# Kernel tuning notes

Measured on AMD Instinct MI355X. Metric: run time of the kernel, lower is better.

The kernel has to match this reference:

```python
import jax, jax.numpy as jnp
import numpy as np
from jax import lax

# ModifiedSRCMLayer dims
B, C, H, W = 4, 128, 64, 64
G, DM = 4, 32          # groups, d_model per group = input_dim // groups
DI, DS, DC = 64, 16, 4 # d_inner = expand*DM, d_state, d_conv
DTR = 2                # dt_rank = ceil(DM/16)
OUT = 128              # output_dim
PE_HW = 64             # sqrt(4096) pos_embed grid
EPS = 1e-5


def setup_inputs() -> dict:
    key = jax.random.key(0)
    ks = jax.random.split(key, 16)
    def n(k, shape, s=0.02):
        return jax.random.normal(k, shape, jnp.float32) * s
    inp = {}
    inp["x"] = jax.random.normal(ks[0], (B, C, H, W), jnp.float32)
    # ConvPosEnc: depthwise 3x3
    inp["pos_conv_w"] = n(ks[1], (C, 1, 3, 3))
    inp["pos_conv_b"] = jnp.zeros((C,), jnp.float32)
    inp["pos_embed"] = jax.random.normal(ks[2], (1, PE_HW * PE_HW, C), jnp.float32)  # torch.randn init
    inp["ln_g"] = jnp.ones((C,), jnp.float32)
    inp["ln_b"] = jnp.zeros((C,), jnp.float32)
    inp["gate_W"] = n(ks[3], (C, C))
    inp["gate_b"] = jnp.zeros((C,), jnp.float32)
    inp["proj_W"] = n(ks[4], (OUT, C))
    inp["proj_b"] = jnp.zeros((OUT,), jnp.float32)
    # per-group bidirectional Mamba (bimamba v2) params; axis0=group, axis1=direction
    inp["m_Win"] = n(ks[5], (G, 2 * DI, DM))
    inp["m_Wout"] = n(ks[6], (G, DM, DI))
    inp["conv_w"] = n(ks[7], (G, 2, DI, DC))
    inp["conv_b"] = jnp.zeros((G, 2, DI), jnp.float32)
    inp["xproj_W"] = n(ks[8], (G, 2, DTR + 2 * DS, DI))
    inp["dt_W"] = n(ks[9], (G, 2, DI, DTR), 0.1)
    inp["dt_b"] = n(ks[10], (G, 2, DI), 0.1)
    A = jnp.log(jnp.tile(jnp.arange(1, DS + 1, dtype=jnp.float32)[None, :], (DI, 1)))  # S4D-real init
    inp["A_log"] = jnp.tile(A[None, None], (G, 2, 1, 1))
    inp["Dskip"] = jnp.ones((G, 2, DI), jnp.float32)
    return inp


def _causal_dwconv(x, w, b):
    # x: (B,L,DI), w: (DI,DC) depthwise causal conv along L
    xt = x.transpose(0, 2, 1)  # (B,DI,L)
    y = lax.conv_general_dilated(xt, w[:, None, :], (1,), [(DC - 1, 0)],
                                 feature_group_count=DI,
                                 dimension_numbers=('NCH', 'OIH', 'NCH'))
    return (y + b[None, :, None]).transpose(0, 2, 1)


def _selective_scan(u, dt, Bm, Cm, A, D):
    # u, dt: (B,L,DI); Bm, Cm: (B,L,DS); A: (DI,DS); D: (DI,)
    def step(h, inp):
        u_t, dt_t, B_t, C_t = inp  # (B,DI),(B,DI),(B,DS),(B,DS)
        dA = jnp.exp(dt_t[:, :, None] * A)                       # (B,DI,DS)
        h = dA * h + (dt_t * u_t)[:, :, None] * B_t[:, None, :]
        return h, jnp.einsum('bds,bs->bd', h, C_t)
    xs = (u.transpose(1, 0, 2), dt.transpose(1, 0, 2),
          Bm.transpose(1, 0, 2), Cm.transpose(1, 0, 2))
    h0 = jnp.zeros((u.shape[0], DI, DS), u.dtype)
    _, ys = lax.scan(step, h0, xs)  # (L,B,DI)
    return ys.transpose(1, 0, 2) + u * D


def _mamba_dir(u, z, conv_w, conv_b, xproj_W, dt_W, dt_b, A_log, D):
    uc = jax.nn.silu(_causal_dwconv(u, conv_w, conv_b))
    dbl = uc @ xproj_W.T                                  # (B,L,DTR+2*DS)
    dt, Bm, Cm = jnp.split(dbl, [DTR, DTR + DS], axis=-1)
    dt = jax.nn.softplus(dt @ dt_W.T + dt_b)              # (B,L,DI)
    y = _selective_scan(uc, dt, Bm, Cm, -jnp.exp(A_log), D)
    return y * jax.nn.silu(z)


def _conv_mamba(xg, Win, Wout, conv_w, conv_b, xproj_W, dt_W, dt_b, A_log, D):
    # xg: (B,L,DM); bidirectional (bimamba v2): fwd scan + flipped scan, summed
    xz = xg @ Win.T
    u, z = jnp.split(xz, 2, axis=-1)
    yf = _mamba_dir(u, z, conv_w[0], conv_b[0], xproj_W[0], dt_W[0], dt_b[0], A_log[0], D[0])
    yb = _mamba_dir(u[:, ::-1], z[:, ::-1], conv_w[1], conv_b[1], xproj_W[1],
                    dt_W[1], dt_b[1], A_log[1], D[1])[:, ::-1]
    return (yf + yb) @ Wout.T


def reference(x, pos_conv_w, pos_conv_b, pos_embed, ln_g, ln_b, gate_W, gate_b,
              proj_W, proj_b, m_Win, m_Wout, conv_w, conv_b, xproj_W, dt_W,
              dt_b, A_log, Dskip):
    Bsz, Cc, Hh, Ww = x.shape
    L = Hh * Ww
    # ConvPosEnc: x + depthwise 3x3
    pe = lax.conv_general_dilated(x, pos_conv_w, (1, 1), [(1, 1), (1, 1)],
                                  feature_group_count=Cc,
                                  dimension_numbers=('NCHW', 'OIHW', 'NCHW'))
    x = x + pe + pos_conv_b[None, :, None, None]
    xs = x.reshape(Bsz, Cc, L).transpose(0, 2, 1)  # (B,L,C)
    # bilinear pos_embed interpolation (align_corners=False == half-pixel 'linear')
    pemb = pos_embed.transpose(0, 2, 1).reshape(1, Cc, PE_HW, PE_HW)
    pemb = jax.image.resize(pemb, (1, Cc, Hh, Ww), 'linear')
    xs = xs + pemb.reshape(1, Cc, L).transpose(0, 2, 1)
    # LayerNorm over channels
    mu = xs.mean(-1, keepdims=True)
    var = ((xs - mu) ** 2).mean(-1, keepdims=True)
    xn = (xs - mu) * lax.rsqrt(var + EPS) * ln_g + ln_b
    # split into G channel groups, run ConvMamba per group (vmapped)
    chunks = xn.reshape(Bsz, L, G, DM).transpose(2, 0, 1, 3)  # (G,B,L,DM)
    ym = jax.vmap(_conv_mamba)(chunks, m_Win, m_Wout, conv_w, conv_b,
                               xproj_W, dt_W, dt_b, A_log, Dskip)  # (G,B,L,DM)
    x_mamba = ym.transpose(1, 2, 0, 3).reshape(Bsz, L, Cc)
    gate = jax.nn.sigmoid(xn @ gate_W.T + gate_b)
    out = gate * x_mamba + (1.0 - gate) * xs
    out = out @ proj_W.T + proj_b
    return out.transpose(0, 2, 1).reshape(Bsz, OUT, Hh, Ww)
```

## Files before the change

kernel.cpp:

```cpp
#include <hip/hip_runtime.h>
#include <hip/hip_bf16.h>
#include <hip/hip_fp16.h>

#define NS 128
#define CL 32

__global__ __launch_bounds__(256) void k1a_conv(
    const float* __restrict__ x, const float* __restrict__ pcw,
    const float* __restrict__ pcb, const float* __restrict__ pemb,
    float* __restrict__ xs)
{
  const int h = blockIdx.x;
  const int b = blockIdx.y >> 2;
  const int c0 = (blockIdx.y & 3) * 32;
  const int tid = threadIdx.x;
  __shared__ float tile[32][65];
  for (int i = 0; i < 8; ++i) {
    int e = tid + 256*i;
    int c = e >> 6, w = e & 63;
    const float* xp = x + ((size_t)(b*128 + c0 + c))*4096;
    const float* wp = pcw + (c0 + c)*9;
    float acc = xp[h*64 + w] + pcb[c0 + c];
    #pragma unroll
    for (int dh = -1; dh <= 1; ++dh) {
      int hh = h + dh;
      if (hh < 0 || hh >= 64) continue;
      #pragma unroll
      for (int dw = -1; dw <= 1; ++dw) {
        int ww = w + dw;
        if (ww < 0 || ww >= 64) continue;
        acc += xp[hh*64 + ww] * wp[(dh+1)*3 + (dw+1)];
      }
    }
    tile[c][w] = acc;
  }
  __syncthreads();
  for (int i = 0; i < 8; ++i) {
    int e = tid + 256*i;
    int w = e >> 5, cc = e & 31;
    int l = h*64 + w;
    xs[((size_t)(b*4096 + l))*128 + c0 + cc] =
        tile[cc][w] + pemb[(size_t)l*128 + c0 + cc];
  }
}

__global__ __launch_bounds__(256) void k1b_ln(
    const float* __restrict__ xs, const float* __restrict__ lng,
    const float* __restrict__ lnb, float* __restrict__ xn)
{
  const int tid = threadIdx.x;
  const int r = tid >> 5, lane = tid & 31;
  const size_t row = (size_t)(blockIdx.x*8 + r);
  const size_t base = row*128 + lane*4;
  float4 v = *(const float4*)&xs[base];
  float sum = v.x + v.y + v.z + v.w;
  float ss  = v.x*v.x + v.y*v.y + v.z*v.z + v.w*v.w;
  sum += __shfl_xor(sum, 1);  ss += __shfl_xor(ss, 1);
  sum += __shfl_xor(sum, 2);  ss += __shfl_xor(ss, 2);
  sum += __shfl_xor(sum, 4);  ss += __shfl_xor(ss, 4);
  sum += __shfl_xor(sum, 8);  ss += __shfl_xor(ss, 8);
  sum += __shfl_xor(sum, 16); ss += __shfl_xor(ss, 16);
  float mu = sum * (1.f/128.f);
  float rs = rsqrtf(ss * (1.f/128.f) - mu*mu + 1e-5f);
  float4 g = *(const float4*)&lng[lane*4];
  float4 be = *(const float4*)&lnb[lane*4];
  float4 o;
  o.x = (v.x - mu)*rs*g.x + be.x;
  o.y = (v.y - mu)*rs*g.y + be.y;
  o.z = (v.z - mu)*rs*g.z + be.z;
  o.w = (v.w - mu)*rs*g.w + be.w;
  *(float4*)&xn[base] = o;
}

__global__ __launch_bounds__(256) void k23_xz_conv_xproj(
    const float* __restrict__ xn, const float* __restrict__ mWin,
    const float* __restrict__ convw, const float* __restrict__ convb,
    const float* __restrict__ xprojW,
    float* __restrict__ uc, float* __restrict__ dtB, float* __restrict__ Cb)
{
  const int l0 = blockIdx.x * 32;
  const int gb = blockIdx.y;
  const int g = gb >> 2, b = gb & 3;
  const int tid = threadIdx.x;
  const int d = tid & 63, t4 = tid >> 6;

  __shared__ float xn_s[38][36];
  __shared__ float u_s[38][68];
  __shared__ float uc_s[32][68];
  __shared__ float xw_s[34][68];

  for (int i = 0; i < 2; ++i) {
    int e = tid + 256*i;
    if (e < 304) {
      int rr = e >> 3, q = e & 7;
      int gr = l0 - 3 + rr;
      float4 v = make_float4(0.f, 0.f, 0.f, 0.f);
      if (gr >= 0 && gr < 4096)
        v = *(const float4*)&xn[((size_t)(b*4096 + gr))*128 + g*32 + q*4];
      *(float4*)&xn_s[rr][q*4] = v;
    }
  }
  float wu[32];
  {
    const float* wr = mWin + (size_t)(g*128 + d)*32;
    #pragma unroll
    for (int q = 0; q < 8; ++q)
      ((float4*)wu)[q] = *(const float4*)&wr[q*4];
  }
  __syncthreads();
  for (int ii = 0; ii < 10; ++ii) {
    int r = t4 + 4*ii;
    if (r < 38) {
      float au = 0.f;
      #pragma unroll
      for (int k4 = 0; k4 < 8; ++k4) {
        float4 a4 = *(const float4*)&xn_s[r][k4*4];
        float4 w4 = ((float4*)wu)[k4];
        au += a4.x*w4.x + a4.y*w4.y + a4.z*w4.z + a4.w*w4.w;
      }
      u_s[r][d] = au;
    }
  }

  for (int dir = 0; dir < 2; ++dir) {
    __syncthreads();
    {
      int g2 = g*2 + dir;
      float4 w4 = *(const float4*)&convw[(g2*64 + d)*4];
      float bb = convb[g2*64 + d];
      float* ucg = uc + ((size_t)(g2*4 + b)*4096)*64;
      #pragma unroll
      for (int ii = 0; ii < 8; ++ii) {
        int r = t4 + 4*ii;
        float acc;
        if (dir == 0)
          acc = bb + u_s[r  ][d]*w4.x + u_s[r+1][d]*w4.y
                   + u_s[r+2][d]*w4.z + u_s[r+3][d]*w4.w;
        else
          acc = bb + u_s[r+3][d]*w4.w + u_s[r+4][d]*w4.z
                   + u_s[r+5][d]*w4.y + u_s[r+6][d]*w4.x;
        acc = acc / (1.f + __expf(-acc));
        uc_s[r][d] = acc;
        int t = l0 + r;
        int tw = dir ? 4095 - t : t;
        ucg[(size_t)tw*64 + d] = acc;
      }
    }
    for (int i = 0; i < 3; ++i) {
      int e = tid + 256*i;
      if (e < 544) {
        int row = e >> 4, q = e & 15;
        *(float4*)&xw_s[row][q*4] =
          *(const float4*)&xprojW[((size_t)((g*2 + dir)*34 + row))*64 + q*4];
      }
    }
    __syncthreads();
    {
      const int rg = tid >> 3, cg = tid & 7;
      float acc[5] = {};
      #pragma unroll
      for (int k4 = 0; k4 < 16; ++k4) {
        float4 u0 = *(const float4*)&uc_s[rg][k4*4];
        #pragma unroll
        for (int j = 0; j < 4; ++j) {
          float4 w = *(const float4*)&xw_s[cg + 8*j][k4*4];
          acc[j] += u0.x*w.x + u0.y*w.y + u0.z*w.z + u0.w*w.w;
        }
        if (cg < 2) {
          float4 w = *(const float4*)&xw_s[32 + cg][k4*4];
          acc[4] += u0.x*w.x + u0.y*w.y + u0.z*w.z + u0.w*w.w;
        }
      }
      int gdb = (g*2 + dir)*4 + b;
      float* dtBg = dtB + ((size_t)gdb*4096)*20;
      float* Cbg  = Cb  + ((size_t)gdb*4096)*16;
      int t = l0 + rg;
      int tw = dir ? 4095 - t : t;
      #pragma unroll
      for (int j = 0; j < 4; ++j) {
        int c = cg + 8*j;
        if (c < 2)       dtBg[(size_t)tw*20 + c] = acc[j];
        else if (c < 18) dtBg[(size_t)tw*20 + 2 + c] = acc[j];
        else             Cbg[(size_t)tw*16 + (c - 18)] = acc[j];
      }
      if (cg < 2) Cbg[(size_t)tw*16 + 14 + cg] = acc[4];
    }
  }
}

__global__ __launch_bounds__(256) void k_scan1y(
    const float* __restrict__ dtB, const float* __restrict__ Cb,
    float* __restrict__ uc,
    const float* __restrict__ dtW, const float* __restrict__ dtb_,
    const float* __restrict__ Dsk, __half* __restrict__ ecum,
    float* __restrict__ hseed, float* __restrict__ eprod)
{
  const int chunk = blockIdx.x;
  const int gdb = blockIdx.y;
  const int g2 = gdb >> 2;
  const int tid = threadIdx.x;
  const int d = tid >> 2, sq = tid & 3, s0 = sq*4;
  const int dld = tid & 63;

  __shared__ float  E_s[2][8][64];
  __shared__ __align__(16) float2 duu_s[2][8][64];
  __shared__ __align__(16) float  bc_s[2][8][32];
  __shared__ float  y_st[2][8][64];
  __shared__ float  e_st[2][8][64];

  float* ucg = uc + ((size_t)gdb*4096)*64;
  const float* dtBg = dtB + ((size_t)gdb*4096)*20;
  const float* Cbg  = Cb  + ((size_t)gdb*4096)*16;
  const int base = chunk * CL;
  __half* eg = ecum + ((size_t)gdb*4096 + base)*64;

  const float dtw0 = dtW[(g2*64 + dld)*2 + 0];
  const float dtw1 = dtW[(g2*64 + dld)*2 + 1];
  const float dtbv = dtb_[g2*64 + dld];
  const float Dd = Dsk[g2*64 + d];

  float h0=0.f,h1=0.f,h2=0.f,h3=0.f, Ec=1.f;

  float pu0, pu1, pc;
  float2 pq0, pq1;
  auto issue = [&](int t0) {
    int ttA = tid >> 6;
    pu0 = ucg[(size_t)(t0+ttA)*64 + dld];
    pq0 = *(const float2*)&dtBg[(size_t)(t0+ttA)*20];
    pu1 = ucg[(size_t)(t0+ttA+4)*64 + dld];
    pq1 = *(const float2*)&dtBg[(size_t)(t0+ttA+4)*20];
    int col = tid & 31, row = t0 + (tid >> 5);
    pc = (col < 16) ? dtBg[(size_t)row*20 + 4 + col]
                    : Cbg[(size_t)row*16 + (col - 16)];
  };
  auto commit = [&](int buf) {
    int ttA = tid >> 6;
    #pragma unroll
    for (int half = 0; half < 2; ++half) {
      int tt = ttA + 4*half;
      float uu = half ? pu1 : pu0;
      float2 pq = half ? pq1 : pq0;
      float v = pq.x*dtw0 + pq.y*dtw1 + dtbv;
      float dt, E;
      if (v > 20.f) { dt = v; E = __expf(-v); }
      else {
        float e = __expf(v);
        dt = __logf(1.f + e);
        E = 1.f / (1.f + e);
      }
      E_s[buf][tt][dld] = E;
      duu_s[buf][tt][dld] = make_float2(dt*uu, uu);
    }
    bc_s[buf][tid>>5][tid&31] = pc;
  };

  issue(base);
  commit(0);
  __syncthreads();
  #pragma unroll 1
  for (int cc = 0; cc < CL/8; ++cc) {
    const int buf = cc & 1;
    const int t0 = base + cc*8;
    if (cc + 1 < CL/8) issue(t0 + 8);
    if (cc > 0) {
      int r = tid >> 6, dd = tid & 63;
      int tp = cc*8 - 8;
      ucg[(size_t)(base+tp+r)*64 + dd]   = y_st[buf^1][r][dd];
      ucg[(size_t)(base+tp+r+4)*64 + dd] = y_st[buf^1][r+4][dd];
      eg[(size_t)(tp+r)*64 + dd]   = __float2half(e_st[buf^1][r][dd]);
      eg[(size_t)(tp+r+4)*64 + dd] = __float2half(e_st[buf^1][r+4][dd]);
    }
    #pragma unroll
    for (int tt = 0; tt < 8; ++tt) {
      float E = E_s[buf][tt][d];
      float E2 = E*E, E4 = E2*E2, E8 = E4*E4;
      float dA0 = E;
      if (sq & 1) dA0 *= E4;
      if (sq & 2) dA0 *= E8;
      float dA1 = dA0*E, dA2 = dA0*E2, dA3 = dA1*E2;
      float2 duu = duu_s[buf][tt][d];
      float4 Bv = *(const float4*)&bc_s[buf][tt][s0];
      h0 = dA0*h0 + duu.x*Bv.x;
      h1 = dA1*h1 + duu.x*Bv.y;
      h2 = dA2*h2 + duu.x*Bv.z;
      h3 = dA3*h3 + duu.x*Bv.w;
      float4 Cv = *(const float4*)&bc_s[buf][tt][16 + s0];
      float p = h0*Cv.x + h1*Cv.y + h2*Cv.z + h3*Cv.w;
      p += __shfl_xor(p, 1);
      p += __shfl_xor(p, 2);
      Ec *= E;
      if (sq == 0) y_st[buf][tt][d] = p + Dd*duu.y;
      else if (sq == 1) e_st[buf][tt][d] = Ec;
    }
    if (cc + 1 < CL/8) commit(buf ^ 1);
    __syncthreads();
  }
  {
    int r = tid >> 6, dd = tid & 63;
    int tp = CL - 8;
    ucg[(size_t)(base+tp+r)*64 + dd]   = y_st[1][r][dd];
    ucg[(size_t)(base+tp+r+4)*64 + dd] = y_st[1][r+4][dd];
    eg[(size_t)(tp+r)*64 + dd]   = __float2half(e_st[1][r][dd]);
    eg[(size_t)(tp+r+4)*64 + dd] = __float2half(e_st[1][r+4][dd]);
  }
  *(float4*)&hseed[(size_t)((gdb*NS + chunk)*64 + d)*16 + s0] =
      make_float4(h0,h1,h2,h3);
  if (sq == 0) eprod[(gdb*NS + chunk)*64 + d] = Ec;
}

__global__ __launch_bounds__(256) void k_scan_fix(
    float* __restrict__ hseed, const float* __restrict__ eprod)
{
  const int gdb = blockIdx.x;
  const int tid = threadIdx.x;
  const int d = tid >> 2, sq = tid & 3, s0 = sq*4;
  float h0=0.f,h1=0.f,h2=0.f,h3=0.f;
  for (int i = 0; i < NS; ++i) {
    int idx = (gdb*NS + i)*64 + d;
    float4 ho = *(const float4*)&hseed[(size_t)idx*16 + s0];
    float E = eprod[idx];
    *(float4*)&hseed[(size_t)idx*16 + s0] = make_float4(h0,h1,h2,h3);
    float E2 = E*E, E4 = E2*E2, E8 = E4*E4;
    float dA0 = E;
    if (sq & 1) dA0 *= E4;
    if (sq & 2) dA0 *= E8;
    float dA1 = dA0*E, dA2 = dA0*E2, dA3 = dA1*E2;
    h0 = dA0*h0 + ho.x;
    h1 = dA1*h1 + ho.y;
    h2 = dA2*h2 + ho.z;
    h3 = dA3*h3 + ho.w;
  }
}

__global__ __launch_bounds__(256) void kC_finish(
    const float* __restrict__ xn, const float* __restrict__ mWin,
    const float* __restrict__ mWout, const float* __restrict__ yv,
    const __half* __restrict__ ecum, const float* __restrict__ Cb,
    const float* __restrict__ hseed, float* __restrict__ xm)
{
  const int l0 = blockIdx.x * 32;
  const int gb = blockIdx.y;
  const int g = gb >> 2, b = gb & 3;
  const int gdb0 = (g*2+0)*4 + b;
  const int gdb1 = (g*2+1)*4 + b;
  const int ch0 = l0 >> 5;
  const int ch1 = (NS-1) - ch0;
  const int tid = threadIdx.x;
  const int d = tid & 63, t4 = tid >> 6;

  __shared__ float vt_s[32*68];
  __shared__ float wo_s[32*68];
  __shared__ float c0_s[32*16];
  __shared__ float c1_s[32*16];
  __shared__ float xn_s[32*36];

  if (tid < 128) {
    int rr = tid >> 2, q = tid & 3;
    *(float4*)&c0_s[rr*16+q*4] =
        *(const float4*)&Cb[((size_t)gdb0*4096 + l0+rr)*16 + q*4];
    *(float4*)&c1_s[rr*16+q*4] =
        *(const float4*)&Cb[((size_t)gdb1*4096 + (4095-(l0+rr)))*16 + q*4];
  }
  {
    int rr = tid >> 3, q = tid & 7;
    *(float4*)&xn_s[rr*36+q*4] =
        *(const float4*)&xn[((size_t)(b*4096+l0+rr))*128 + g*32 + q*4];
  }
  for (int e = tid; e < 512; e += 256) {
    int m = e >> 4, q = e & 15;
    *(float4*)&wo_s[m*68 + q*4] = *(const float4*)&mWout[((size_t)(g*32+m))*64 + q*4];
  }
  float hr0[16], hr1[16];
  {
    const float* hp0 = &hseed[((size_t)(gdb0*NS + ch0)*64 + d)*16];
    const float* hp1 = &hseed[((size_t)(gdb1*NS + ch1)*64 + d)*16];
    #pragma unroll
    for (int q = 0; q < 4; ++q) {
      ((float4*)hr0)[q] = *(const float4*)&hp0[q*4];
      ((float4*)hr1)[q] = *(const float4*)&hp1[q*4];
    }
  }
  float wz[32];
  {
    const float* zr = mWin + (size_t)(g*128 + 64 + d)*32;
    #pragma unroll
    for (int q = 0; q < 8; ++q) ((float4*)wz)[q] = *(const float4*)&zr[q*4];
  }
  __syncthreads();
  #pragma unroll
  for (int ii = 0; ii < 8; ++ii) {
    int rl = t4 + 4*ii;
    size_t r0 = (size_t)gdb0*4096 + (size_t)(l0 + rl);
    size_t r1 = (size_t)gdb1*4096 + (size_t)(4095 - (l0 + rl));
    float zv = 0.f;
    #pragma unroll
    for (int k4 = 0; k4 < 8; ++k4) {
      float4 a4 = *(const float4*)&xn_s[rl*36 + k4*4];
      float4 w4 = ((float4*)wz)[k4];
      zv += a4.x*w4.x + a4.y*w4.y + a4.z*w4.z + a4.w*w4.w;
    }
    float sz = zv / (1.f + __expf(-zv));
    float E0 = __half2float(ecum[r0*64 + d]);
    float E1 = __half2float(ecum[r1*64 + d]);
    float yy = yv[r0*64 + d] + yv[r1*64 + d];
    float a0 = 0.f, a1 = 0.f;
    #pragma unroll
    for (int s = 15; s >= 0; --s) {
      a0 = a0*E0 + c0_s[rl*16+s]*hr0[s];
      a1 = a1*E1 + c1_s[rl*16+s]*hr1[s];
    }
    vt_s[rl*68+d] = (yy + a0*E0 + a1*E1) * sz;
  }
  __syncthreads();
  {
    const int m = tid & 31, rg = tid >> 5;
    float acc[4] = {};
    #pragma unroll
    for (int k4 = 0; k4 < 16; ++k4) {
      float4 w4 = *(const float4*)&wo_s[m*68 + k4*4];
      #pragma unroll
      for (int rr2 = 0; rr2 < 4; ++rr2) {
        float4 a = *(const float4*)&vt_s[(rg + 8*rr2)*68 + k4*4];
        acc[rr2] += a.x*w4.x + a.y*w4.y + a.z*w4.z + a.w*w4.w;
      }
    }
    #pragma unroll
    for (int rr2 = 0; rr2 < 4; ++rr2)
      xm[((size_t)(b*4096 + l0 + rg + 8*rr2))*128 + g*32 + m] = acc[rr2];
  }
}

__global__ __launch_bounds__(256) void k6_final(
    const float* __restrict__ xn, const float* __restrict__ xs,
    const float* __restrict__ xm, const float* __restrict__ gateW,
    const float* __restrict__ gateb, const float* __restrict__ projW,
    const float* __restrict__ projb, float* __restrict__ out)
{
  const int l0 = blockIdx.x * 32;
  const int b = blockIdx.y;
  const int tid = threadIdx.x;
  __shared__ float a[32][132];
  __shared__ float wT[32][129];
  const int rg = tid >> 5, cg = tid & 31;

  for (int i = 0; i < 16; ++i) {
    int e = tid + 256*i;
    int r = e >> 7, c = e & 127;
    a[r][c] = xn[((size_t)(b*4096 + l0 + r))*128 + c];
  }
  __syncthreads();

  float ac[4][4] = {};
  for (int kb = 0; kb < 4; ++kb) {
    if (kb) __syncthreads();
    for (int i = 0; i < 16; ++i) {
      int e = tid + 256*i;
      int c = e >> 5, kk = e & 31;
      wT[kk][c] = gateW[c*128 + kb*32 + kk];
    }
    __syncthreads();
    #pragma unroll
    for (int k4 = 0; k4 < 8; ++k4) {
      float4 a4[4];
      #pragma unroll
      for (int rr = 0; rr < 4; ++rr)
        a4[rr] = *(const float4*)&a[rg + 8*rr][kb*32 + k4*4];
      #pragma unroll
      for (int q = 0; q < 4; ++q) {
        int kk = k4*4 + q;
        float w0 = wT[kk][cg], w1 = wT[kk][cg+32],
              w2 = wT[kk][cg+64], w3 = wT[kk][cg+96];
        #pragma unroll
        for (int rr = 0; rr < 4; ++rr) {
          float av = (q==0) ? a4[rr].x : (q==1) ? a4[rr].y : (q==2) ? a4[rr].z : a4[rr].w;
          ac[rr][0] += av*w0; ac[rr][1] += av*w1;
          ac[rr][2] += av*w2; ac[rr][3] += av*w3;
        }
      }
    }
  }
  float mix[4][4];
  #pragma unroll
  for (int rr = 0; rr < 4; ++rr) {
    size_t row = ((size_t)(b*4096 + l0 + rg + 8*rr))*128;
    #pragma unroll
    for (int j = 0; j < 4; ++j) {
      int c = cg + 32*j;
      float gt = 1.f / (1.f + __expf(-(ac[rr][j] + gateb[c])));
      float xsv = xs[row + c], xmv = xm[row + c];
      mix[rr][j] = xsv + gt*(xmv - xsv);
    }
  }
  __syncthreads();
  #pragma unroll
  for (int rr = 0; rr < 4; ++rr)
    #pragma unroll
    for (int j = 0; j < 4; ++j)
      a[rg + 8*rr][cg + 32*j] = mix[rr][j];
  __syncthreads();

  float ap[4][4] = {};
  for (int kb = 0; kb < 4; ++kb) {
    if (kb) __syncthreads();
    for (int i = 0; i < 16; ++i) {
      int e = tid + 256*i;
      int c = e >> 5, kk = e & 31;
      wT[kk][c] = projW[c*128 + kb*32 + kk];
    }
    __syncthreads();
    #pragma unroll
    for (int k4 = 0; k4 < 8; ++k4) {
      float4 a4[4];
      #pragma unroll
      for (int rr = 0; rr < 4; ++rr)
        a4[rr] = *(const float4*)&a[rg + 8*rr][kb*32 + k4*4];
      #pragma unroll
      for (int q = 0; q < 4; ++q) {
        int kk = k4*4 + q;
        float w0 = wT[kk][cg], w1 = wT[kk][cg+32],
              w2 = wT[kk][cg+64], w3 = wT[kk][cg+96];
        #pragma unroll
        for (int rr = 0; rr < 4; ++rr) {
          float av = (q==0) ? a4[rr].x : (q==1) ? a4[rr].y : (q==2) ? a4[rr].z : a4[rr].w;
          ap[rr][0] += av*w0; ap[rr][1] += av*w1;
          ap[rr][2] += av*w2; ap[rr][3] += av*w3;
        }
      }
    }
  }
  __syncthreads();
  float* at = &a[0][0];
  #pragma unroll
  for (int rr = 0; rr < 4; ++rr)
    #pragma unroll
    for (int j = 0; j < 4; ++j) {
      int o = cg + 32*j;
      at[o*33 + rg + 8*rr] = ap[rr][j] + projb[o];
    }
  __syncthreads();
  for (int i = 0; i < 16; ++i) {
    int e = tid + 256*i;
    int o = e >> 5, ll = e & 31;
    out[((size_t)(b*128 + o))*4096 + l0 + ll] = at[o*33 + ll];
  }
}

extern "C" void kernel_launch(void* const* d_in, const int* in_sizes, int n_in,
                              void* d_out, int out_size, void* d_ws, size_t ws_size,
                              hipStream_t stream) {
  const float* x      = (const float*)d_in[0];
  const float* pcw    = (const float*)d_in[1];
  const float* pcb    = (const float*)d_in[2];
  const float* pemb   = (const float*)d_in[3];
  const float* lng    = (const float*)d_in[4];
  const float* lnb    = (const float*)d_in[5];
  const float* gateW  = (const float*)d_in[6];
  const float* gateb  = (const float*)d_in[7];
  const float* projW  = (const float*)d_in[8];
  const float* projb  = (const float*)d_in[9];
  const float* mWin   = (const float*)d_in[10];
  const float* mWout  = (const float*)d_in[11];
  const float* convw  = (const float*)d_in[12];
  const float* convb  = (const float*)d_in[13];
  const float* xprojW = (const float*)d_in[14];
  const float* dtW    = (const float*)d_in[15];
  const float* dtb    = (const float*)d_in[16];
  const float* Dsk    = (const float*)d_in[18];
  float* out = (float*)d_out;

  float* ws = (float*)d_ws;
  float* xs    = ws;
  float* xn    = xs + 2097152;
  float* uc    = xn + 2097152;
  float* dtB   = uc + 8388608;
  float* Cb    = dtB + 2621440;
  float* xm    = Cb + 2097152;
  float* hseed = xm + 2097152;
  float* eprod = hseed + 4194304;
  __half* ecum = (__half*)(eprod + 262144);

  k1a_conv<<<dim3(64, 16), 256, 0, stream>>>(x, pcw, pcb, pemb, xs);
  k1b_ln<<<dim3(2048), 256, 0, stream>>>(xs, lng, lnb, xn);
  k23_xz_conv_xproj<<<dim3(128, 16), 256, 0, stream>>>(
      xn, mWin, convw, convb, xprojW, uc, dtB, Cb);
  k_scan1y<<<dim3(NS, 32), 256, 0, stream>>>(
      dtB, Cb, uc, dtW, dtb, Dsk, ecum, hseed, eprod);
  k_scan_fix<<<dim3(32), 256, 0, stream>>>(hseed, eprod);
  kC_finish<<<dim3(128, 16), 256, 0, stream>>>(
      xn, mWin, mWout, uc, ecum, Cb, hseed, xm);
  k6_final<<<dim3(128, 4), 256, 0, stream>>>(xn, xs, xm, gateW, gateb, projW, projb, out);
}
```

Measured before the change: 270.3 us.

## Warp-specialize chunk scan into producer loader and consumer scan warps

Splits the per-chunk selective-scan kernel so threads 128-255 act as producers that load inputs, compute dt/E and stage them in shared memory, and later write back outputs. Threads 0-127 act as consumers that run the recurrence with 8 states per thread instead of 4, using one shuffle instead of two. The aim is to overlap global loads and stores with the serial scan and to vectorize loads and stores. Only half the threads now do scan arithmetic, which lengthens each consumer's serial chain, and the block barrier schedule is changed.

```diff
diff --git a/kernel.cpp b/kernel.cpp
--- a/kernel.cpp
+++ b/kernel.cpp
@@ -199,8 +199,7 @@
   const int gdb = blockIdx.y;
   const int g2 = gdb >> 2;
   const int tid = threadIdx.x;
-  const int d = tid >> 2, sq = tid & 3, s0 = sq*4;
-  const int dld = tid & 63;
+  const int base = chunk * CL;
 
   __shared__ float  E_s[2][8][64];
   __shared__ __align__(16) float2 duu_s[2][8][64];
@@ -211,101 +210,102 @@
   float* ucg = uc + ((size_t)gdb*4096)*64;
   const float* dtBg = dtB + ((size_t)gdb*4096)*20;
   const float* Cbg  = Cb  + ((size_t)gdb*4096)*16;
-  const int base = chunk * CL;
   __half* eg = ecum + ((size_t)gdb*4096 + base)*64;
 
-  const float dtw0 = dtW[(g2*64 + dld)*2 + 0];
-  const float dtw1 = dtW[(g2*64 + dld)*2 + 1];
-  const float dtbv = dtb_[g2*64 + dld];
-  const float Dd = Dsk[g2*64 + d];
-
-  float h0=0.f,h1=0.f,h2=0.f,h3=0.f, Ec=1.f;
-
-  float pu0, pu1, pc;
-  float2 pq0, pq1;
-  auto issue = [&](int t0) {
-    int ttA = tid >> 6;
-    pu0 = ucg[(size_t)(t0+ttA)*64 + dld];
-    pq0 = *(const float2*)&dtBg[(size_t)(t0+ttA)*20];
-    pu1 = ucg[(size_t)(t0+ttA+4)*64 + dld];
-    pq1 = *(const float2*)&dtBg[(size_t)(t0+ttA+4)*20];
-    int col = tid & 31, row = t0 + (tid >> 5);
-    pc = (col < 16) ? dtBg[(size_t)row*20 + 4 + col]
-                    : Cbg[(size_t)row*16 + (col - 16)];
-  };
-  auto commit = [&](int buf) {
-    int ttA = tid >> 6;
-    #pragma unroll
-    for (int half = 0; half < 2; ++half) {
-      int tt = ttA + 4*half;
-      float uu = half ? pu1 : pu0;
-      float2 pq = half ? pq1 : pq0;
-      float v = pq.x*dtw0 + pq.y*dtw1 + dtbv;
-      float dt, E;
-      if (v > 20.f) { dt = v; E = __expf(-v); }
-      else {
-        float e = __expf(v);
-        dt = __logf(1.f + e);
-        E = 1.f / (1.f + e);
-      }
-      E_s[buf][tt][dld] = E;
-      duu_s[buf][tt][dld] = make_float2(dt*uu, uu);
-    }
-    bc_s[buf][tid>>5][tid&31] = pc;
-  };
-
-  issue(base);
-  commit(0);
-  __syncthreads();
-  #pragma unroll 1
-  for (int cc = 0; cc < CL/8; ++cc) {
-    const int buf = cc & 1;
-    const int t0 = base + cc*8;
-    if (cc + 1 < CL/8) issue(t0 + 8);
-    if (cc > 0) {
-      int r = tid >> 6, dd = tid & 63;
-      int tp = cc*8 - 8;
-      ucg[(size_t)(base+tp+r)*64 + dd]   = y_st[buf^1][r][dd];
-      ucg[(size_t)(base+tp+r+4)*64 + dd] = y_st[buf^1][r+4][dd];
-      eg[(size_t)(tp+r)*64 + dd]   = __float2half(e_st[buf^1][r][dd]);
-      eg[(size_t)(tp+r+4)*64 + dd] = __float2half(e_st[buf^1][r+4][dd]);
-    }
-    #pragma unroll
-    for (int tt = 0; tt < 8; ++tt) {
-      float E = E_s[buf][tt][d];
-      float E2 = E*E, E4 = E2*E2, E8 = E4*E4;
-      float dA0 = E;
-      if (sq & 1) dA0 *= E4;
-      if (sq & 2) dA0 *= E8;
-      float dA1 = dA0*E, dA2 = dA0*E2, dA3 = dA1*E2;
-      float2 duu = duu_s[buf][tt][d];
-      float4 Bv = *(const float4*)&bc_s[buf][tt][s0];
-      h0 = dA0*h0 + duu.x*Bv.x;
-      h1 = dA1*h1 + duu.x*Bv.y;
-      h2 = dA2*h2 + duu.x*Bv.z;
-      h3 = dA3*h3 + duu.x*Bv.w;
-      float4 Cv = *(const float4*)&bc_s[buf][tt][16 + s0];
-      float p = h0*Cv.x + h1*Cv.y + h2*Cv.z + h3*Cv.w;
-      p += __shfl_xor(p, 1);
-      p += __shfl_xor(p, 2);
-      Ec *= E;
-      if (sq == 0) y_st[buf][tt][d] = p + Dd*duu.y;
-      else if (sq == 1) e_st[buf][tt][d] = Ec;
-    }
-    if (cc + 1 < CL/8) commit(buf ^ 1);
+  if (tid >= 128) {
+    const int j = tid - 128;
+    const int row = j >> 4;
+    const int q = j & 15;
+    const int d0 = q*4;
+    float dtw0[4], dtw1[4], dtbv[4];
+    #pragma unroll
+    for (int k = 0; k < 4; ++k) {
+      dtw0[k] = dtW[(g2*64 + d0+k)*2 + 0];
+      dtw1[k] = dtW[(g2*64 + d0+k)*2 + 1];
+      dtbv[k] = dtb_[g2*64 + d0+k];
+    }
+    auto fill = [&](int buf, int t0) {
+      int t = t0 + row;
+      float4 u4 = *(const float4*)&ucg[(size_t)t*64 + d0];
+      float2 pq = *(const float2*)&dtBg[(size_t)t*20];
+      float Bv = dtBg[(size_t)t*20 + 4 + q];
+      float Cv = Cbg[(size_t)t*16 + q];
+      float uu4[4] = {u4.x, u4.y, u4.z, u4.w};
+      float E4v[4], du4[4];
+      #pragma unroll
+      for (int k = 0; k < 4; ++k) {
+        float v = pq.x*dtw0[k] + pq.y*dtw1[k] + dtbv[k];
+        float dt, E;
+        if (v > 20.f) { dt = v; E = __expf(-v); }
+        else { float e = __expf(v); dt = __logf(1.f+e); E = 1.f/(1.f+e); }
+        E4v[k] = E;
+        du4[k] = dt*uu4[k];
+      }
+      *(float4*)&E_s[buf][row][d0] = make_float4(E4v[0],E4v[1],E4v[2],E4v[3]);
+      #pragma unroll
+      for (int k = 0; k < 4; ++k)
+        duu_s[buf][row][d0+k] = make_float2(du4[k], uu4[k]);
+      bc_s[buf][row][q] = Bv;
+      bc_s[buf][row][16+q] = Cv;
+    };
+    auto drain = [&](int buf, int t0) {
+      int t = t0 + row;
+      *(float4*)&ucg[(size_t)t*64 + d0] = *(const float4*)&y_st[buf][row][d0];
+      float4 ev = *(const float4*)&e_st[buf][row][d0];
+      __half2* ep = (__half2*)&eg[(size_t)(t - base)*64 + d0];
+      ep[0] = __halves2half2(__float2half(ev.x), __float2half(ev.y));
+      ep[1] = __halves2half2(__float2half(ev.z), __float2half(ev.w));
+    };
+    fill(0, base);
     __syncthreads();
-  }
-  {
-    int r = tid >> 6, dd = tid & 63;
-    int tp = CL - 8;
-    ucg[(size_t)(base+tp+r)*64 + dd]   = y_st[1][r][dd];
-    ucg[(size_t)(base+tp+r+4)*64 + dd] = y_st[1][r+4][dd];
-    eg[(size_t)(tp+r)*64 + dd]   = __float2half(e_st[1][r][dd]);
-    eg[(size_t)(tp+r+4)*64 + dd] = __float2half(e_st[1][r+4][dd]);
-  }
-  *(float4*)&hseed[(size_t)((gdb*NS + chunk)*64 + d)*16 + s0] =
-      make_float4(h0,h1,h2,h3);
-  if (sq == 0) eprod[(gdb*NS + chunk)*64 + d] = Ec;
+    for (int cc = 0; cc < CL/8; ++cc) {
+      if (cc + 1 < CL/8) fill((cc&1)^1, base + (cc+1)*8);
+      if (cc > 0) drain((cc&1)^1, base + (cc-1)*8);
+      __syncthreads();
+    }
+    drain((CL/8-1)&1, base + CL - 8);
+  } else {
+    const int d = tid >> 1, hi = tid & 1, s0 = 8*hi;
+    const float Dd = Dsk[g2*64 + d];
+    float h[8];
+    #pragma unroll
+    for (int k = 0; k < 8; ++k) h[k] = 0.f;
+    float Ec = 1.f;
+    __syncthreads();
+    for (int cc = 0; cc < CL/8; ++cc) {
+      const int buf = cc & 1;
+      #pragma unroll
+      for (int tt = 0; tt < 8; ++tt) {
+        float E = E_s[buf][tt][d];
+        float2 duu = duu_s[buf][tt][d];
+        float4 Bv0 = *(const float4*)&bc_s[buf][tt][s0];
+        float4 Bv1 = *(const float4*)&bc_s[buf][tt][s0+4];
+        float4 Cv0 = *(const float4*)&bc_s[buf][tt][16+s0];
+        float4 Cv1 = *(const float4*)&bc_s[buf][tt][16+s0+4];
+        float E2 = E*E, E4 = E2*E2, E8 = E4*E4;
+        float dA = hi ? E8*E : E;
+        float du = duu.x;
+        float p;
+        h[0] = dA*h[0] + du*Bv0.x; p  = h[0]*Cv0.x; dA *= E;
+        h[1] = dA*h[1] + du*Bv0.y; p += h[1]*Cv0.y; dA *= E;
+        h[2] = dA*h[2] + du*Bv0.z; p += h[2]*Cv0.z; dA *= E;
+        h[3] = dA*h[3] + du*Bv0.w; p += h[3]*Cv0.w; dA *= E;
+        h[4] = dA*h[4] + du*Bv1.x; p += h[4]*Cv1.x; dA *= E;
+        h[5] = dA*h[5] + du*Bv1.y; p += h[5]*Cv1.y; dA *= E;
+        h[6] = dA*h[6] + du*Bv1.z; p += h[6]*Cv1.z; dA *= E;
+        h[7] = dA*h[7] + du*Bv1.w; p += h[7]*Cv1.w;
+        p += __shfl_xor(p, 1);
+        Ec *= E;
+        if (hi == 0) y_st[buf][tt][d] = p + Dd*duu.y;
+        else         e_st[buf][tt][d] = Ec;
+      }
+      __syncthreads();
+    }
+    float* hp = &hseed[((size_t)((gdb*NS + chunk)*64 + d))*16 + s0];
+    *(float4*)&hp[0] = make_float4(h[0],h[1],h[2],h[3]);
+    *(float4*)&hp[4] = make_float4(h[4],h[5],h[6],h[7]);
+    if (hi == 0) eprod[(gdb*NS + chunk)*64 + d] = Ec;
+  }
 }
 
 __global__ __launch_bounds__(256) void k_scan_fix(
```

Result: faster. 258.2 us (-4.5%).
